# Performance work log

Measured on AMD Instinct MI355X. Metric: run time of the kernel, lower is better.

Reference implementation:

```python
import jax, jax.numpy as jnp
import numpy as np
import math

IN_DIM = 4096
OUT_DIM = 4096
BLOCK_SIZE = 64
RECT_NUM = 128
DEPTH = 3
PADDED_DIM = 4096  # 2**ceil(log2(in_dim)); in_dim is already a power of 2 -> pad = 0
NUM_BLOCK_GROUPS = PADDED_DIM // BLOCK_SIZE  # 64
BLOCK_WIDTH = PADDED_DIM // RECT_NUM         # 32
BLOCK_HEIGHT = OUT_DIM // RECT_NUM           # 32


def fwht(x):
    """Fast Walsh-Hadamard transform along last dim. x: [B, D], D power of 2."""
    B, D = x.shape
    h = 1
    while h < D:  # static loop, log2(D) iterations
        x = x.reshape(B, D // (2 * h), 2, h)
        a = x[:, :, 0, :]
        b = x[:, :, 1, :]
        x = jnp.stack([a + b, a - b], axis=2).reshape(B, D)
        h *= 2
    return x


def setup_inputs() -> dict:
    key = jax.random.key(0)
    k1, k2, k3 = jax.random.split(key, 3)
    x = jax.random.normal(k1, (4, 4096, IN_DIM), dtype=jnp.float32)
    # inner_B: (depth-1) block-diagonal stages, stacked: [depth-1, num_block_groups, bs, bs]
    inner_B = jax.random.normal(k2, (DEPTH - 1, NUM_BLOCK_GROUPS, BLOCK_SIZE, BLOCK_SIZE), dtype=jnp.float32)
    final_B = 0.1 * jax.random.normal(k3, (RECT_NUM, BLOCK_WIDTH, BLOCK_HEIGHT), dtype=jnp.float32)
    return {"x": x, "inner_B": inner_B, "final_B": final_B}


def reference(x, inner_B, final_B):
    orig_shape = x.shape
    xf = x.reshape(-1, IN_DIM)  # pad == 0, so padded view == flattened view
    B = xf.shape[0]
    scale = 1.0 / math.sqrt(PADDED_DIM)
    for i in range(inner_B.shape[0]):  # static loop over depth-1 butterfly stages
        xb = xf.reshape(B, NUM_BLOCK_GROUPS, BLOCK_SIZE)
        xb = jnp.einsum('bni,nio->bno', xb, inner_B[i])
        xf = fwht(xb.reshape(B, PADDED_DIM)) * scale
    xr = xf.reshape(B, RECT_NUM, BLOCK_WIDTH)
    out = jnp.einsum('bni,nio->bno', xr, final_B)
    return out.reshape(*orig_shape[:-1], OUT_DIM)
```

## Files before the change

kernel.cpp:

```cpp
#include <hip/hip_runtime.h>
#include <hip/hip_bf16.h>


typedef __attribute__((ext_vector_type(8))) short bf16x8;
typedef __attribute__((ext_vector_type(4))) short bf16x4;
typedef __attribute__((ext_vector_type(4))) float f32x4;

#define MFMA16(a, b, c) __builtin_amdgcn_mfma_f32_16x16x32_bf16((a), (b), (c), 0, 0, 0)

__device__ __forceinline__ short f2bf(float f) {
    unsigned int u; __builtin_memcpy(&u, &f, 4);
    u += 0x7FFFu + ((u >> 16) & 1u);
    return (short)(u >> 16);
}
__device__ __forceinline__ int swz(int b, int d) {
    int key = (b + (d >> 8)) & 15;
    return (b << 12) | (d & 0xFC0) | ((((d >> 2) & 15) ^ key) << 2) | (d & 3);
}

__global__ __launch_bounds__(256) void prep_inner(const float* __restrict__ B, short* __restrict__ out) {
    int rid  = blockIdx.x * 4 + (threadIdx.x >> 6);
    int lane = threadIdx.x & 63;
    float v = B[rid * 64 + lane];
    #pragma unroll
    for (int m = 1; m < 64; m <<= 1) {
        float p = __shfl_xor(v, m, 64);
        v = (lane & m) ? (p - v) : (v + p);
    }
    int l = rid >> 12, g = (rid >> 6) & 63, j = rid & 63;
    int o = lane;
    int jj = j & 7, lhi = (j >> 3) & 3, ks = j >> 5;
    int it = o >> 4;
    int lane_dst = lhi * 16 + (o & 15);
    int fid = l * 512 + g * 8 + it * 2 + ks;
    out[(fid * 64 + lane_dst) * 8 + jj] = f2bf(v * 0.015625f);
}

__global__ void prep_final(const float* __restrict__ F, short* __restrict__ out) {
    int e = blockIdx.x * 256 + threadIdx.x;
    int ww = e & 7, lane = (e >> 3) & 63, fid = e >> 9;
    int ot = fid & 1, r = fid >> 1;
    int w = ((lane >> 4) << 3) + ww;
    int o = ot * 16 + (lane & 15);
    out[e] = f2bf(F[(r * 32 + w) * 32 + o]);
}

__global__ __launch_bounds__(1024, 4) void bh_main(
        const float* __restrict__ Xg,
        const short* __restrict__ CW,
        const short* __restrict__ FW,
        float* __restrict__ Og) {
    __shared__ short sm[16 * 4096];
    const int tid  = threadIdx.x;
    const int lane = tid & 63;
    const int wave = tid >> 6;
    const long row0 = (long)blockIdx.x * 16;

    bf16x8 Hf[2][4];
    {
        int n0 = lane & 15, mb = (lane >> 4) << 3;
        #pragma unroll
        for (int ks = 0; ks < 2; ++ks)
            #pragma unroll
            for (int nt = 0; nt < 4; ++nt) {
                bf16x8 h;
                #pragma unroll
                for (int jj = 0; jj < 8; ++jj) {
                    int m = ks * 32 + mb + jj, n = nt * 16 + n0;
                    h[jj] = (short)((__builtin_popcount(m & n) & 1) ? 0xBF80 : 0x3F80);
                }
                Hf[ks][nt] = h;
            }
    }

    {
        const float* src = Xg + row0 * 4096;
        const int d   = (tid & 511) * 8;
        const int bb0 = (tid >> 9) * 8;
        #pragma unroll
        for (int bb = 0; bb < 8; ++bb) {
            int b = bb0 + bb;
            f32x4 v0 = *(const f32x4*)(src + (long)b * 4096 + d);
            f32x4 v1 = *(const f32x4*)(src + (long)b * 4096 + d + 4);
            bf16x4 q0 = { f2bf(v0[0]), f2bf(v0[1]), f2bf(v0[2]), f2bf(v0[3]) };
            bf16x4 q1 = { f2bf(v1[0]), f2bf(v1[1]), f2bf(v1[2]), f2bf(v1[3]) };
            *(bf16x4*)(sm + swz(b, d))     = q0;
            *(bf16x4*)(sm + swz(b, d + 4)) = q1;
        }
    }
    __syncthreads();

    #pragma unroll 1
    for (int l = 0; l < 2; ++l) {
        {
            const int b = lane & 15;
            const int koff = (lane >> 4) << 3;
            const short* Wl = CW + l * 262144;
            #pragma unroll 2
            for (int gi = 0; gi < 4; ++gi) {
                int g = wave * 4 + gi;
                bf16x8 wf[4][2];
                #pragma unroll
                for (int it = 0; it < 4; ++it)
                    #pragma unroll
                    for (int ks = 0; ks < 2; ++ks)
                        wf[it][ks] = *(const bf16x8*)(Wl + ((g * 8 + it * 2 + ks) * 64 + lane) * 8);
                bf16x8 xf[2];
                #pragma unroll
                for (int ks = 0; ks < 2; ++ks) {
                    int d = g * 64 + ks * 32 + koff;
                    bf16x4 a0 = *(const bf16x4*)(sm + swz(b, d));
                    bf16x4 a1 = *(const bf16x4*)(sm + swz(b, d + 4));
                    xf[ks] = bf16x8{a0[0],a0[1],a0[2],a0[3],a1[0],a1[1],a1[2],a1[3]};
                }
                #pragma unroll
                for (int it = 0; it < 4; ++it) {
                    f32x4 acc = {0.f, 0.f, 0.f, 0.f};
                    acc = MFMA16(wf[it][0], xf[0], acc);
                    acc = MFMA16(wf[it][1], xf[1], acc);
                    int i0 = it * 16 + ((lane >> 4) << 2);
                    bf16x4 o4 = { f2bf(acc[0]), f2bf(acc[1]), f2bf(acc[2]), f2bf(acc[3]) };
                    *(bf16x4*)(sm + swz(b, g * 64 + i0)) = o4;
                }
            }
        }
        __syncthreads();

        {
            const int ba = lane & 15;
            const int moff = (lane >> 4) << 3;
            const int i0 = wave << 2;
            bf16x4 rd[2][8];
            #pragma unroll
            for (int ks = 0; ks < 2; ++ks)
                #pragma unroll
                for (int mm = 0; mm < 8; ++mm)
                    rd[ks][mm] = *(const bf16x4*)(sm + swz(ba, (ks * 32 + moff + mm) * 64 + i0));
            f32x4 acc[4][4];
            #pragma unroll
            for (int c = 0; c < 4; ++c) {
                bf16x8 af0, af1;
                #pragma unroll
                for (int mm = 0; mm < 8; ++mm) { af0[mm] = rd[0][mm][c]; af1[mm] = rd[1][mm][c]; }
                #pragma unroll
                for (int nt = 0; nt < 4; ++nt) {
                    f32x4 a = {0.f, 0.f, 0.f, 0.f};
                    a = MFMA16(af0, Hf[0][nt], a);
                    a = MFMA16(af1, Hf[1][nt], a);
                    acc[c][nt] = a;
                }
            }
            const int n0 = lane & 15;
            const int bq = (lane >> 4) << 2;
            #pragma unroll
            for (int nt = 0; nt < 4; ++nt) {
                int n = nt * 16 + n0;
                #pragma unroll
                for (int q = 0; q < 4; ++q) {
                    int b = bq + q;
                    bf16x4 o4 = { f2bf(acc[0][nt][q]), f2bf(acc[1][nt][q]),
                                  f2bf(acc[2][nt][q]), f2bf(acc[3][nt][q]) };
                    *(bf16x4*)(sm + swz(b, n * 64 + i0)) = o4;
                }
            }
        }
        __syncthreads();
    }

    {
        const int b = lane & 15;
        const int woff = (lane >> 4) << 3;
        float* Orow = Og + (row0 + b) * 4096;
        #pragma unroll 2
        for (int ri = 0; ri < 8; ++ri) {
            int r = wave * 8 + ri;
            bf16x8 wf0 = *(const bf16x8*)(FW + ((r * 2 + 0) * 64 + lane) * 8);
            bf16x8 wf1 = *(const bf16x8*)(FW + ((r * 2 + 1) * 64 + lane) * 8);
            int d = r * 32 + woff;
            bf16x4 a0 = *(const bf16x4*)(sm + swz(b, d));
            bf16x4 a1 = *(const bf16x4*)(sm + swz(b, d + 4));
            bf16x8 xf = {a0[0],a0[1],a0[2],a0[3],a1[0],a1[1],a1[2],a1[3]};
            #pragma unroll
            for (int ot = 0; ot < 2; ++ot) {
                f32x4 acc = {0.f, 0.f, 0.f, 0.f};
                acc = MFMA16(ot ? wf1 : wf0, xf, acc);
                int o0 = ot * 16 + ((lane >> 4) << 2);
                *(f32x4*)(Orow + r * 32 + o0) = acc;
            }
        }
    }
}

extern "C" void kernel_launch(void* const* d_in, const int* in_sizes, int n_in,
                              void* d_out, int out_size, void* d_ws, size_t ws_size,
                              hipStream_t stream) {
    const float* x  = (const float*)d_in[0];
    const float* iB = (const float*)d_in[1];
    const float* fB = (const float*)d_in[2];
    short* CW = (short*)d_ws;
    short* FW = CW + 524288;

    prep_inner<<<2048, 256, 0, stream>>>(iB, CW);
    prep_final<<<512, 256, 0, stream>>>(fB, FW);
    bh_main<<<1024, 1024, 0, stream>>>(x, CW, FW, (float*)d_out);
}
```

Baseline: 588.8 us.

## Make main kernel persistent over four row tiles with register-prefetched input

The main kernel now launches 256 workgroups of 512 threads. Each workgroup loops over four 16-row tiles and prefetches the first half of the next tile's fp32 input into registers while the current tile's butterfly stages run. Barriers become a custom wait-plus-s_barrier macro, and each wave handles twice as many groups per stage. The aim is to hide global load latency behind compute and cut launch and barrier overhead, at the cost of higher register pressure and fewer waves in flight per CU.

```diff
diff --git a/kernel.cpp b/kernel.cpp
--- a/kernel.cpp
+++ b/kernel.cpp
@@ -7,6 +7,11 @@
 typedef __attribute__((ext_vector_type(4))) float f32x4;
 
 #define MFMA16(a, b, c) __builtin_amdgcn_mfma_f32_16x16x32_bf16((a), (b), (c), 0, 0, 0)
+
+#define WG_SYNC() do { \
+    asm volatile("s_waitcnt lgkmcnt(0)" ::: "memory"); \
+    __builtin_amdgcn_s_barrier(); \
+} while (0)
 
 __device__ __forceinline__ short f2bf(float f) {
     unsigned int u; __builtin_memcpy(&u, &f, 4);
@@ -45,7 +50,7 @@
     out[e] = f2bf(F[(r * 32 + w) * 32 + o]);
 }
 
-__global__ __launch_bounds__(1024, 4) void bh_main(
+__global__ __launch_bounds__(512, 2) void bh_main(
         const float* __restrict__ Xg,
         const short* __restrict__ CW,
         const short* __restrict__ FW,
@@ -54,7 +59,7 @@
     const int tid  = threadIdx.x;
     const int lane = tid & 63;
     const int wave = tid >> 6;
-    const long row0 = (long)blockIdx.x * 16;
+    const int d8   = tid * 8;
 
     bf16x8 Hf[2][4];
     {
@@ -73,121 +78,159 @@
             }
     }
 
+    f32x4 P[16];
     {
+        const float* src0 = Xg + (long)blockIdx.x * 64 * 4096;
+        #pragma unroll
+        for (int b = 0; b < 8; ++b) {
+            P[2*b]   = *(const f32x4*)(src0 + (long)b * 4096 + d8);
+            P[2*b+1] = *(const f32x4*)(src0 + (long)b * 4096 + d8 + 4);
+        }
+    }
+
+    #pragma unroll 1
+    for (int t = 0; t < 4; ++t) {
+        const long row0 = (long)blockIdx.x * 64 + t * 16;
         const float* src = Xg + row0 * 4096;
-        const int d   = (tid & 511) * 8;
-        const int bb0 = (tid >> 9) * 8;
-        #pragma unroll
-        for (int bb = 0; bb < 8; ++bb) {
-            int b = bb0 + bb;
-            f32x4 v0 = *(const f32x4*)(src + (long)b * 4096 + d);
-            f32x4 v1 = *(const f32x4*)(src + (long)b * 4096 + d + 4);
-            bf16x4 q0 = { f2bf(v0[0]), f2bf(v0[1]), f2bf(v0[2]), f2bf(v0[3]) };
-            bf16x4 q1 = { f2bf(v1[0]), f2bf(v1[1]), f2bf(v1[2]), f2bf(v1[3]) };
-            *(bf16x4*)(sm + swz(b, d))     = q0;
-            *(bf16x4*)(sm + swz(b, d + 4)) = q1;
-        }
-    }
-    __syncthreads();
-
-    #pragma unroll 1
-    for (int l = 0; l < 2; ++l) {
+
+        {
+            f32x4 V[16];
+            #pragma unroll
+            for (int b = 8; b < 16; ++b) {
+                V[2*(b-8)]   = *(const f32x4*)(src + (long)b * 4096 + d8);
+                V[2*(b-8)+1] = *(const f32x4*)(src + (long)b * 4096 + d8 + 4);
+            }
+            #pragma unroll
+            for (int b = 0; b < 8; ++b) {
+                f32x4 v0 = P[2*b], v1 = P[2*b+1];
+                bf16x4 q0 = { f2bf(v0[0]), f2bf(v0[1]), f2bf(v0[2]), f2bf(v0[3]) };
+                bf16x4 q1 = { f2bf(v1[0]), f2bf(v1[1]), f2bf(v1[2]), f2bf(v1[3]) };
+                *(bf16x4*)(sm + swz(b, d8))     = q0;
+                *(bf16x4*)(sm + swz(b, d8 + 4)) = q1;
+            }
+            #pragma unroll
+            for (int b = 8; b < 16; ++b) {
+                f32x4 v0 = V[2*(b-8)], v1 = V[2*(b-8)+1];
+                bf16x4 q0 = { f2bf(v0[0]), f2bf(v0[1]), f2bf(v0[2]), f2bf(v0[3]) };
+                bf16x4 q1 = { f2bf(v1[0]), f2bf(v1[1]), f2bf(v1[2]), f2bf(v1[3]) };
+                *(bf16x4*)(sm + swz(b, d8))     = q0;
+                *(bf16x4*)(sm + swz(b, d8 + 4)) = q1;
+            }
+        }
+        WG_SYNC();
+
+        if (t < 3) {
+            const float* srcn = src + 16 * 4096;
+            #pragma unroll
+            for (int b = 0; b < 8; ++b) {
+                P[2*b]   = *(const f32x4*)(srcn + (long)b * 4096 + d8);
+                P[2*b+1] = *(const f32x4*)(srcn + (long)b * 4096 + d8 + 4);
+            }
+        }
+
+        #pragma unroll 1
+        for (int l = 0; l < 2; ++l) {
+            {
+                const int b = lane & 15;
+                const int koff = (lane >> 4) << 3;
+                const short* Wl = CW + l * 262144;
+                #pragma unroll 2
+                for (int gi = 0; gi < 8; ++gi) {
+                    int g = wave * 8 + gi;
+                    bf16x8 wf[4][2];
+                    #pragma unroll
+                    for (int it = 0; it < 4; ++it)
+                        #pragma unroll
+                        for (int ks = 0; ks < 2; ++ks)
+                            wf[it][ks] = *(const bf16x8*)(Wl + ((g * 8 + it * 2 + ks) * 64 + lane) * 8);
+                    bf16x8 xf[2];
+                    #pragma unroll
+                    for (int ks = 0; ks < 2; ++ks) {
+                        int d = g * 64 + ks * 32 + koff;
+                        bf16x4 a0 = *(const bf16x4*)(sm + swz(b, d));
+                        bf16x4 a1 = *(const bf16x4*)(sm + swz(b, d + 4));
+                        xf[ks] = bf16x8{a0[0],a0[1],a0[2],a0[3],a1[0],a1[1],a1[2],a1[3]};
+                    }
+                    #pragma unroll
+                    for (int it = 0; it < 4; ++it) {
+                        f32x4 acc = {0.f, 0.f, 0.f, 0.f};
+                        acc = MFMA16(wf[it][0], xf[0], acc);
+                        acc = MFMA16(wf[it][1], xf[1], acc);
+                        int i0 = it * 16 + ((lane >> 4) << 2);
+                        bf16x4 o4 = { f2bf(acc[0]), f2bf(acc[1]), f2bf(acc[2]), f2bf(acc[3]) };
+                        *(bf16x4*)(sm + swz(b, g * 64 + i0)) = o4;
+                    }
+                }
+            }
+            WG_SYNC();
+
+            {
+                const int ba = lane & 15;
+                const int moff = (lane >> 4) << 3;
+                #pragma unroll 1
+                for (int s = 0; s < 2; ++s) {
+                    const int i0 = (wave * 2 + s) << 2;
+                    bf16x4 rd[2][8];
+                    #pragma unroll
+                    for (int ks = 0; ks < 2; ++ks)
+                        #pragma unroll
+                        for (int mm = 0; mm < 8; ++mm)
+                            rd[ks][mm] = *(const bf16x4*)(sm + swz(ba, (ks * 32 + moff + mm) * 64 + i0));
+                    f32x4 acc[4][4];
+                    #pragma unroll
+                    for (int c = 0; c < 4; ++c) {
+                        bf16x8 af0, af1;
+                        #pragma unroll
+                        for (int mm = 0; mm < 8; ++mm) { af0[mm] = rd[0][mm][c]; af1[mm] = rd[1][mm][c]; }
+                        #pragma unroll
+                        for (int nt = 0; nt < 4; ++nt) {
+                            f32x4 a = {0.f, 0.f, 0.f, 0.f};
+                            a = MFMA16(af0, Hf[0][nt], a);
+                            a = MFMA16(af1, Hf[1][nt], a);
+                            acc[c][nt] = a;
+                        }
+                    }
+                    const int n0 = lane & 15;
+                    const int bq = (lane >> 4) << 2;
+                    #pragma unroll
+                    for (int nt = 0; nt < 4; ++nt) {
+                        int n = nt * 16 + n0;
+                        #pragma unroll
+                        for (int q = 0; q < 4; ++q) {
+                            int b = bq + q;
+                            bf16x4 o4 = { f2bf(acc[0][nt][q]), f2bf(acc[1][nt][q]),
+                                          f2bf(acc[2][nt][q]), f2bf(acc[3][nt][q]) };
+                            *(bf16x4*)(sm + swz(b, n * 64 + i0)) = o4;
+                        }
+                    }
+                }
+            }
+            WG_SYNC();
+        }
+
         {
             const int b = lane & 15;
-            const int koff = (lane >> 4) << 3;
-            const short* Wl = CW + l * 262144;
+            const int woff = (lane >> 4) << 3;
+            float* Orow = Og + (row0 + b) * 4096;
             #pragma unroll 2
-            for (int gi = 0; gi < 4; ++gi) {
-                int g = wave * 4 + gi;
-                bf16x8 wf[4][2];
+            for (int ri = 0; ri < 16; ++ri) {
+                int r = wave * 16 + ri;
+                bf16x8 wf0 = *(const bf16x8*)(FW + ((r * 2 + 0) * 64 + lane) * 8);
+                bf16x8 wf1 = *(const bf16x8*)(FW + ((r * 2 + 1) * 64 + lane) * 8);
+                int d = r * 32 + woff;
+                bf16x4 a0 = *(const bf16x4*)(sm + swz(b, d));
+                bf16x4 a1 = *(const bf16x4*)(sm + swz(b, d + 4));
+                bf16x8 xf = {a0[0],a0[1],a0[2],a0[3],a1[0],a1[1],a1[2],a1[3]};
                 #pragma unroll
-                for (int it = 0; it < 4; ++it)
-                    #pragma unroll
-                    for (int ks = 0; ks < 2; ++ks)
-                        wf[it][ks] = *(const bf16x8*)(Wl + ((g * 8 + it * 2 + ks) * 64 + lane) * 8);
-                bf16x8 xf[2];
-                #pragma unroll
-                for (int ks = 0; ks < 2; ++ks) {
-                    int d = g * 64 + ks * 32 + koff;
-                    bf16x4 a0 = *(const bf16x4*)(sm + swz(b, d));
-                    bf16x4 a1 = *(const bf16x4*)(sm + swz(b, d + 4));
-                    xf[ks] = bf16x8{a0[0],a0[1],a0[2],a0[3],a1[0],a1[1],a1[2],a1[3]};
-                }
-                #pragma unroll
-                for (int it = 0; it < 4; ++it) {
+                for (int ot = 0; ot < 2; ++ot) {
                     f32x4 acc = {0.f, 0.f, 0.f, 0.f};
-                    acc = MFMA16(wf[it][0], xf[0], acc);
-                    acc = MFMA16(wf[it][1], xf[1], acc);
-                    int i0 = it * 16 + ((lane >> 4) << 2);
-                    bf16x4 o4 = { f2bf(acc[0]), f2bf(acc[1]), f2bf(acc[2]), f2bf(acc[3]) };
-                    *(bf16x4*)(sm + swz(b, g * 64 + i0)) = o4;
-                }
-            }
-        }
-        __syncthreads();
-
-        {
-            const int ba = lane & 15;
-            const int moff = (lane >> 4) << 3;
-            const int i0 = wave << 2;
-            bf16x4 rd[2][8];
-            #pragma unroll
-            for (int ks = 0; ks < 2; ++ks)
-                #pragma unroll
-                for (int mm = 0; mm < 8; ++mm)
-                    rd[ks][mm] = *(const bf16x4*)(sm + swz(ba, (ks * 32 + moff + mm) * 64 + i0));
-            f32x4 acc[4][4];
-            #pragma unroll
-            for (int c = 0; c < 4; ++c) {
-                bf16x8 af0, af1;
-                #pragma unroll
-                for (int mm = 0; mm < 8; ++mm) { af0[mm] = rd[0][mm][c]; af1[mm] = rd[1][mm][c]; }
-                #pragma unroll
-                for (int nt = 0; nt < 4; ++nt) {
-                    f32x4 a = {0.f, 0.f, 0.f, 0.f};
-                    a = MFMA16(af0, Hf[0][nt], a);
-                    a = MFMA16(af1, Hf[1][nt], a);
-                    acc[c][nt] = a;
-                }
-            }
-            const int n0 = lane & 15;
-            const int bq = (lane >> 4) << 2;
-            #pragma unroll
-            for (int nt = 0; nt < 4; ++nt) {
-                int n = nt * 16 + n0;
-                #pragma unroll
-                for (int q = 0; q < 4; ++q) {
-                    int b = bq + q;
-                    bf16x4 o4 = { f2bf(acc[0][nt][q]), f2bf(acc[1][nt][q]),
-                                  f2bf(acc[2][nt][q]), f2bf(acc[3][nt][q]) };
-                    *(bf16x4*)(sm + swz(b, n * 64 + i0)) = o4;
-                }
-            }
-        }
-        __syncthreads();
-    }
-
-    {
-        const int b = lane & 15;
-        const int woff = (lane >> 4) << 3;
-        float* Orow = Og + (row0 + b) * 4096;
-        #pragma unroll 2
-        for (int ri = 0; ri < 8; ++ri) {
-            int r = wave * 8 + ri;
-            bf16x8 wf0 = *(const bf16x8*)(FW + ((r * 2 + 0) * 64 + lane) * 8);
-            bf16x8 wf1 = *(const bf16x8*)(FW + ((r * 2 + 1) * 64 + lane) * 8);
-            int d = r * 32 + woff;
-            bf16x4 a0 = *(const bf16x4*)(sm + swz(b, d));
-            bf16x4 a1 = *(const bf16x4*)(sm + swz(b, d + 4));
-            bf16x8 xf = {a0[0],a0[1],a0[2],a0[3],a1[0],a1[1],a1[2],a1[3]};
-            #pragma unroll
-            for (int ot = 0; ot < 2; ++ot) {
-                f32x4 acc = {0.f, 0.f, 0.f, 0.f};
-                acc = MFMA16(ot ? wf1 : wf0, xf, acc);
-                int o0 = ot * 16 + ((lane >> 4) << 2);
-                *(f32x4*)(Orow + r * 32 + o0) = acc;
-            }
-        }
+                    acc = MFMA16(ot ? wf1 : wf0, xf, acc);
+                    int o0 = ot * 16 + ((lane >> 4) << 2);
+                    *(f32x4*)(Orow + r * 32 + o0) = acc;
+                }
+            }
+        }
+        WG_SYNC();
     }
 }
 
@@ -202,5 +245,5 @@
 
     prep_inner<<<2048, 256, 0, stream>>>(iB, CW);
     prep_final<<<512, 256, 0, stream>>>(fB, FW);
-    bh_main<<<1024, 1024, 0, stream>>>(x, CW, FW, (float*)d_out);
-}
+    bh_main<<<256, 512, 0, stream>>>(x, CW, FW, (float*)d_out);
+}
```

Result: faster. 540.8 us (-8.2%).
